# Performance work log

Hardware: AMD Instinct MI355X
Metric: run time of the kernel (lower is better)

## Reference

```python
import jax, jax.numpy as jnp
import numpy as np

B, H, W = 8, 80, 160
N = B * H * W          # flattened pixels
G = 8                  # cost groups
D = 64                 # disparity candidates
NS = 4                 # num_seed
E = 128                # embed_dim
NFREQ = 15             # fourier freqs -> (2*15+1)*1 = 31 dims
NORMALIZER = 3.14 / 64


def setup_inputs() -> dict:
    key = jax.random.key(0)
    ks = jax.random.split(key, 8)
    cost_volume = jax.random.normal(ks[0], (N, G, D), jnp.float32)
    label_seed = jax.random.randint(ks[1], (N, NS), 0, D)
    context = jax.random.normal(ks[2], (B, H, W, E), jnp.float32)
    s = 0.02
    W1 = jax.random.normal(ks[3], (G * 9, E), jnp.float32) * s
    b1 = jnp.zeros((E,), jnp.float32)
    W2 = jax.random.normal(ks[4], (E, E), jnp.float32) * s
    b2 = jnp.zeros((E,), jnp.float32)
    Wp = jax.random.normal(ks[5], (E + 31, E), jnp.float32) * s
    return {"cost_volume": cost_volume, "label_seed": label_seed, "context": context,
            "W1": W1, "b1": b1, "W2": W2, "b2": b2, "Wp": Wp}


def sample_cost(cost_volume, label_seed):
    # cost_volume: [N,G,D], label_seed: [N,NS] -> [N,NS,G*9]
    offset = jnp.arange(-4, 5, dtype=label_seed.dtype)              # [9]
    idx = jnp.clip(label_seed[:, :, None] + offset, 0, D - 1)      # [N,NS,9]
    idx = jnp.broadcast_to(idx.reshape(N, 1, NS * 9), (N, G, NS * 9))
    cost = jnp.take_along_axis(cost_volume, idx, axis=-1)          # [N,G,NS*9]
    # rearrange 'b h (n c) -> b n (h c)'
    cost = cost.reshape(N, G, NS, 9).transpose(0, 2, 1, 3).reshape(N, NS, G * 9)
    return cost


def fourier_embed(label_f):
    # label_f: [N,NS] float -> [N,NS,31]
    coord = label_f * NORMALIZER                                   # [N,NS]
    freqs = 2.0 ** jnp.arange(NFREQ, dtype=label_f.dtype)          # logscale bands
    f = coord[..., None] * freqs                                   # [N,NS,15]
    return jnp.concatenate([jnp.sin(f), jnp.cos(f), coord[..., None]], axis=-1)


def reference(cost_volume, label_seed, context, W1, b1, W2, b2, Wp):
    cost = sample_cost(cost_volume, label_seed)                    # [N,NS,72]
    h = jax.nn.gelu(cost @ W1 + b1, approximate=False)
    cost_feat = h @ W2 + b2                                        # [N,NS,E]
    label_f = label_seed.astype(jnp.float32)
    disp_enc = fourier_embed(label_f)                              # [N,NS,31]
    sample_embed = jnp.concatenate([cost_feat, disp_enc], axis=-1) @ Wp  # [N,NS,E]
    # layers=[] and norm=None -> passthrough; context unused
    return sample_embed[None], label_f
```

## Files before the change

kernel.cpp:

```cpp
#include <hip/hip_runtime.h>
#include <hip/hip_bf16.h>
#include <math.h>

#define NPIX 102400
#define NSEED 4
#define RTOT (NPIX * NSEED)
#define GG 8
#define DD 64
#define EE 128
#define BM 64

#define KP1 96
#define KP2 128
#define KP3 160

#define PC 104
#define PH 136
#define PF 168

typedef short bf16x8 __attribute__((ext_vector_type(8)));
typedef short bf16x4 __attribute__((ext_vector_type(4)));
typedef float f32x4 __attribute__((ext_vector_type(4)));

static __device__ __forceinline__ short f2bf(float x) {
    __hip_bfloat16 h = __float2bfloat16(x);
    return __builtin_bit_cast(short, h);
}

static __device__ __forceinline__ float gelu_exact(float x) {
    return 0.5f * x * (1.0f + erff(x * 0.7071067811865475f));
}

__global__ void prep_weights(const float* __restrict__ W1,
                             const float* __restrict__ W2,
                             const float* __restrict__ Wp,
                             short* __restrict__ ws) {
    const int i = blockIdx.x * 256 + threadIdx.x;
    if (i < 12288) {
        const int e = i / KP1, k = i - e * KP1;
        ws[i] = (k < 72) ? f2bf(W1[k * EE + e]) : (short)0;
    } else if (i < 12288 + 16384) {
        const int j = i - 12288;
        const int e = j / KP2, k = j - e * KP2;
        ws[i] = f2bf(W2[k * EE + e]);
    } else if (i < 49152) {
        const int j = i - 28672;
        const int e = j / KP3, k = j - e * KP3;
        ws[i] = (k < 159) ? f2bf(Wp[k * EE + e]) : (short)0;
    }
}

template <int KPAD, int PADB>
__device__ __forceinline__ void gemm_tiles(const short* __restrict__ WT, const short* sB,
                                           int mt0, int ln, int qd, f32x4 acc[2][4]) {
#pragma unroll
    for (int ks = 0; ks < KPAD / 32; ++ks) {
        const int kb = ks * 32 + qd * 8;
        const bf16x8 a0 = *(const bf16x8*)(WT + (mt0 * 16 + ln) * KPAD + kb);
        const bf16x8 a1 = *(const bf16x8*)(WT + (mt0 * 16 + 16 + ln) * KPAD + kb);
        const bf16x8 b0 = *(const bf16x8*)(sB + (0 * 16 + ln) * PADB + kb);
        const bf16x8 b1 = *(const bf16x8*)(sB + (1 * 16 + ln) * PADB + kb);
        const bf16x8 b2 = *(const bf16x8*)(sB + (2 * 16 + ln) * PADB + kb);
        const bf16x8 b3 = *(const bf16x8*)(sB + (3 * 16 + ln) * PADB + kb);
        acc[0][0] = __builtin_amdgcn_mfma_f32_16x16x32_bf16(a0, b0, acc[0][0], 0, 0, 0);
        acc[0][1] = __builtin_amdgcn_mfma_f32_16x16x32_bf16(a0, b1, acc[0][1], 0, 0, 0);
        acc[0][2] = __builtin_amdgcn_mfma_f32_16x16x32_bf16(a0, b2, acc[0][2], 0, 0, 0);
        acc[0][3] = __builtin_amdgcn_mfma_f32_16x16x32_bf16(a0, b3, acc[0][3], 0, 0, 0);
        acc[1][0] = __builtin_amdgcn_mfma_f32_16x16x32_bf16(a1, b0, acc[1][0], 0, 0, 0);
        acc[1][1] = __builtin_amdgcn_mfma_f32_16x16x32_bf16(a1, b1, acc[1][1], 0, 0, 0);
        acc[1][2] = __builtin_amdgcn_mfma_f32_16x16x32_bf16(a1, b2, acc[1][2], 0, 0, 0);
        acc[1][3] = __builtin_amdgcn_mfma_f32_16x16x32_bf16(a1, b3, acc[1][3], 0, 0, 0);
    }
}

__global__ __launch_bounds__(256, 4)
void Propagation_85315230368231_kernel(const float* __restrict__ cost_volume,
                                       const int* __restrict__ label_seed,
                                       const short* __restrict__ ws,
                                       const float* __restrict__ b1,
                                       const float* __restrict__ b2,
                                       float* __restrict__ out) {
    __shared__ short sU[BM * PF];
    __shared__ short sHT[BM * PH];
    __shared__ int sSeed[BM];

    const short* W1T = ws;
    const short* W2T = ws + 12288;
    const short* WpT = ws + 28672;

    const int tid = threadIdx.x;
    const int blk = blockIdx.x;
    const int p0 = blk * (BM / NSEED);
    const int row0 = blk * BM;

    const int wave = tid >> 6;
    const int lane = tid & 63;
    const int ln = lane & 15;
    const int qd = lane >> 4;
    const int mt0 = wave * 2;

    if (tid < BM) {
        const int sd = label_seed[row0 + tid];
        sSeed[tid] = sd;
        out[(size_t)RTOT * EE + row0 + tid] = (float)sd;
    }
    __syncthreads();

    for (int e = tid; e < BM * 36; e += 256) {
        const int row = e / 36;
        const int pr = e - row * 36;
        const int k0 = pr * 2, k1 = k0 + 1;
        const int sd = sSeed[row];
        const float* cvn = cost_volume + (size_t)(p0 + (row >> 2)) * (GG * DD);
        const int g0 = k0 / 9, c0 = k0 - g0 * 9;
        int d0 = sd + c0 - 4; d0 = d0 < 0 ? 0 : (d0 > 63 ? 63 : d0);
        const float v0 = cvn[g0 * DD + d0];
        const int g1 = k1 / 9, c1 = k1 - g1 * 9;
        int d1 = sd + c1 - 4; d1 = d1 < 0 ? 0 : (d1 > 63 ? 63 : d1);
        const float v1 = cvn[g1 * DD + d1];
        const int pk = (int)(unsigned short)f2bf(v0) | ((int)(unsigned short)f2bf(v1) << 16);
        *(int*)(sU + row * PC + k0) = pk;
    }
    for (int e = tid; e < BM * 12; e += 256) {
        const int row = e / 12;
        const int j = e - row * 12;
        *(int*)(sU + row * PC + 72 + 2 * j) = 0;
    }
    __syncthreads();

    f32x4 acc[2][4];

#pragma unroll
    for (int i = 0; i < 2; ++i)
#pragma unroll
        for (int j = 0; j < 4; ++j) acc[i][j] = (f32x4)0.0f;
    gemm_tiles<KP1, PC>(W1T, sU, mt0, ln, qd, acc);
#pragma unroll
    for (int mi = 0; mi < 2; ++mi) {
        const int eb = (mt0 + mi) * 16 + qd * 4;
        const float4 bv = *(const float4*)(b1 + eb);
#pragma unroll
        for (int nt = 0; nt < 4; ++nt) {
            bf16x4 p;
            p[0] = f2bf(gelu_exact(acc[mi][nt][0] + bv.x));
            p[1] = f2bf(gelu_exact(acc[mi][nt][1] + bv.y));
            p[2] = f2bf(gelu_exact(acc[mi][nt][2] + bv.z));
            p[3] = f2bf(gelu_exact(acc[mi][nt][3] + bv.w));
            *(bf16x4*)(sHT + (nt * 16 + ln) * PH + eb) = p;
        }
    }
    __syncthreads();

    for (int e = tid; e < BM * 32; e += 256) {
        const int row = e >> 5;
        const int j = e & 31;
        const float coord = (float)sSeed[row] * (float)(3.14 / 64.0);
        float v;
        if (j < 15) v = sinf(coord * (float)(1 << j));
        else if (j < 30) v = cosf(coord * (float)(1 << (j - 15)));
        else if (j == 30) v = coord;
        else v = 0.0f;
        sU[row * PF + 128 + j] = f2bf(v);
    }

#pragma unroll
    for (int i = 0; i < 2; ++i)
#pragma unroll
        for (int j = 0; j < 4; ++j) acc[i][j] = (f32x4)0.0f;
    gemm_tiles<KP2, PH>(W2T, sHT, mt0, ln, qd, acc);
#pragma unroll
    for (int mi = 0; mi < 2; ++mi) {
        const int eb = (mt0 + mi) * 16 + qd * 4;
        const float4 bv = *(const float4*)(b2 + eb);
#pragma unroll
        for (int nt = 0; nt < 4; ++nt) {
            bf16x4 p;
            p[0] = f2bf(acc[mi][nt][0] + bv.x);
            p[1] = f2bf(acc[mi][nt][1] + bv.y);
            p[2] = f2bf(acc[mi][nt][2] + bv.z);
            p[3] = f2bf(acc[mi][nt][3] + bv.w);
            *(bf16x4*)(sU + (nt * 16 + ln) * PF + eb) = p;
        }
    }
    __syncthreads();

#pragma unroll
    for (int i = 0; i < 2; ++i)
#pragma unroll
        for (int j = 0; j < 4; ++j) acc[i][j] = (f32x4)0.0f;
    gemm_tiles<KP3, PF>(WpT, sU, mt0, ln, qd, acc);
#pragma unroll
    for (int mi = 0; mi < 2; ++mi) {
        const int eb = (mt0 + mi) * 16 + qd * 4;
#pragma unroll
        for (int nt = 0; nt < 4; ++nt) {
            const size_t grow = (size_t)(row0 + nt * 16 + ln);
            float4 v = {acc[mi][nt][0], acc[mi][nt][1], acc[mi][nt][2], acc[mi][nt][3]};
            *(float4*)(out + grow * EE + eb) = v;
        }
    }
}

extern "C" void kernel_launch(void* const* d_in, const int* in_sizes, int n_in,
                              void* d_out, int out_size, void* d_ws, size_t ws_size,
                              hipStream_t stream) {
    const float* cost_volume = (const float*)d_in[0];
    const int* label_seed = (const int*)d_in[1];
    const float* W1 = (const float*)d_in[3];
    const float* b1 = (const float*)d_in[4];
    const float* W2 = (const float*)d_in[5];
    const float* b2 = (const float*)d_in[6];
    const float* Wp = (const float*)d_in[7];
    float* out = (float*)d_out;
    short* ws = (short*)d_ws;

    prep_weights<<<192, 256, 0, stream>>>(W1, W2, Wp, ws);
    Propagation_85315230368231_kernel<<<RTOT / BM, 256, 0, stream>>>(
        cost_volume, label_seed, ws, b1, b2, out);
}
```

Baseline: 461.3 us.

## Restructure MLP kernel to per-wave 16-row tiles with register-resident operands

Each wave now handles its own 16 rows end to end. The gathered cost values are built directly in registers as MFMA B operands, and a private per-wave LDS slice replaces block-wide __syncthreads. The Fourier disparity embedding is precomputed into a 64-entry table in the prep kernel, biases are folded into the accumulator initialisation, outputs use nontemporal stores, and exact erf GELU is replaced by a sigmoid approximation. Together these remove block barriers and transcendental work, but the GELU approximation changes numerics and may exceed tolerance.

```diff
diff --git a/kernel.cpp b/kernel.cpp
--- a/kernel.cpp
+++ b/kernel.cpp
@@ -2,74 +2,52 @@
 #include <hip/hip_bf16.h>
 #include <math.h>
 
-#define NPIX 102400
 #define NSEED 4
-#define RTOT (NPIX * NSEED)
-#define GG 8
-#define DD 64
+#define RTOT 409600
 #define EE 128
-#define BM 64
-
 #define KP1 96
 #define KP2 128
 #define KP3 160
-
-#define PC 104
 #define PH 136
-#define PF 168
 
 typedef short bf16x8 __attribute__((ext_vector_type(8)));
-typedef short bf16x4 __attribute__((ext_vector_type(4)));
 typedef float f32x4 __attribute__((ext_vector_type(4)));
+typedef int   i32x4 __attribute__((ext_vector_type(4)));
 
 static __device__ __forceinline__ short f2bf(float x) {
     __hip_bfloat16 h = __float2bfloat16(x);
     return __builtin_bit_cast(short, h);
 }
 
-static __device__ __forceinline__ float gelu_exact(float x) {
-    return 0.5f * x * (1.0f + erff(x * 0.7071067811865475f));
+static __device__ __forceinline__ int pack2(float a, float b) {
+    return (int)(unsigned short)f2bf(a) | ((int)(unsigned short)f2bf(b) << 16);
 }
 
-__global__ void prep_weights(const float* __restrict__ W1,
-                             const float* __restrict__ W2,
-                             const float* __restrict__ Wp,
-                             short* __restrict__ ws) {
+static __device__ __forceinline__ float gelu_fast(float x) {
+    return x / (1.0f + __expf(-1.702f * x));
+}
+
+__global__ void prep_tables(const float* __restrict__ W1, const float* __restrict__ W2,
+                            const float* __restrict__ Wp, short* __restrict__ ws) {
     const int i = blockIdx.x * 256 + threadIdx.x;
     if (i < 12288) {
         const int e = i / KP1, k = i - e * KP1;
         ws[i] = (k < 72) ? f2bf(W1[k * EE + e]) : (short)0;
-    } else if (i < 12288 + 16384) {
-        const int j = i - 12288;
-        const int e = j / KP2, k = j - e * KP2;
+    } else if (i < 28672) {
+        const int j = i - 12288; const int e = j >> 7, k = j & 127;
         ws[i] = f2bf(W2[k * EE + e]);
     } else if (i < 49152) {
-        const int j = i - 28672;
-        const int e = j / KP3, k = j - e * KP3;
+        const int j = i - 28672; const int e = j / KP3, k = j - e * KP3;
         ws[i] = (k < 159) ? f2bf(Wp[k * EE + e]) : (short)0;
-    }
-}
-
-template <int KPAD, int PADB>
-__device__ __forceinline__ void gemm_tiles(const short* __restrict__ WT, const short* sB,
-                                           int mt0, int ln, int qd, f32x4 acc[2][4]) {
-#pragma unroll
-    for (int ks = 0; ks < KPAD / 32; ++ks) {
-        const int kb = ks * 32 + qd * 8;
-        const bf16x8 a0 = *(const bf16x8*)(WT + (mt0 * 16 + ln) * KPAD + kb);
-        const bf16x8 a1 = *(const bf16x8*)(WT + (mt0 * 16 + 16 + ln) * KPAD + kb);
-        const bf16x8 b0 = *(const bf16x8*)(sB + (0 * 16 + ln) * PADB + kb);
-        const bf16x8 b1 = *(const bf16x8*)(sB + (1 * 16 + ln) * PADB + kb);
-        const bf16x8 b2 = *(const bf16x8*)(sB + (2 * 16 + ln) * PADB + kb);
-        const bf16x8 b3 = *(const bf16x8*)(sB + (3 * 16 + ln) * PADB + kb);
-        acc[0][0] = __builtin_amdgcn_mfma_f32_16x16x32_bf16(a0, b0, acc[0][0], 0, 0, 0);
-        acc[0][1] = __builtin_amdgcn_mfma_f32_16x16x32_bf16(a0, b1, acc[0][1], 0, 0, 0);
-        acc[0][2] = __builtin_amdgcn_mfma_f32_16x16x32_bf16(a0, b2, acc[0][2], 0, 0, 0);
-        acc[0][3] = __builtin_amdgcn_mfma_f32_16x16x32_bf16(a0, b3, acc[0][3], 0, 0, 0);
-        acc[1][0] = __builtin_amdgcn_mfma_f32_16x16x32_bf16(a1, b0, acc[1][0], 0, 0, 0);
-        acc[1][1] = __builtin_amdgcn_mfma_f32_16x16x32_bf16(a1, b1, acc[1][1], 0, 0, 0);
-        acc[1][2] = __builtin_amdgcn_mfma_f32_16x16x32_bf16(a1, b2, acc[1][2], 0, 0, 0);
-        acc[1][3] = __builtin_amdgcn_mfma_f32_16x16x32_bf16(a1, b3, acc[1][3], 0, 0, 0);
+    } else if (i < 51200) {
+        const int j = i - 49152; const int sd = j >> 5, jj = j & 31;
+        const float coord = (float)sd * (float)(3.14 / 64.0);
+        float v;
+        if (jj < 15) v = sinf(coord * (float)(1 << jj));
+        else if (jj < 30) v = cosf(coord * (float)(1 << (jj - 15)));
+        else if (jj == 30) v = coord;
+        else v = 0.0f;
+        ws[i] = f2bf(v);
     }
 }
 
@@ -80,124 +58,118 @@
                                        const float* __restrict__ b1,
                                        const float* __restrict__ b2,
                                        float* __restrict__ out) {
-    __shared__ short sU[BM * PF];
-    __shared__ short sHT[BM * PH];
-    __shared__ int sSeed[BM];
+    __shared__ short sH[4][16 * PH];
 
     const short* W1T = ws;
     const short* W2T = ws + 12288;
     const short* WpT = ws + 28672;
+    const short* DSP = ws + 49152;
 
     const int tid = threadIdx.x;
-    const int blk = blockIdx.x;
-    const int p0 = blk * (BM / NSEED);
-    const int row0 = blk * BM;
-
     const int wave = tid >> 6;
     const int lane = tid & 63;
     const int ln = lane & 15;
     const int qd = lane >> 4;
-    const int mt0 = wave * 2;
+    short* sHw = sH[wave];
 
-    if (tid < BM) {
-        const int sd = label_seed[row0 + tid];
-        sSeed[tid] = sd;
-        out[(size_t)RTOT * EE + row0 + tid] = (float)sd;
+    const int gw = blockIdx.x * 4 + wave;
+    const int row0 = gw * 16;
+    const int row = row0 + ln;
+    const int n = row >> 2;
+
+    const int sd = label_seed[row];
+    if (qd == 0) {
+        __builtin_nontemporal_store((float)sd, out + (size_t)RTOT * EE + row);
     }
-    __syncthreads();
 
-    for (int e = tid; e < BM * 36; e += 256) {
-        const int row = e / 36;
-        const int pr = e - row * 36;
-        const int k0 = pr * 2, k1 = k0 + 1;
-        const int sd = sSeed[row];
-        const float* cvn = cost_volume + (size_t)(p0 + (row >> 2)) * (GG * DD);
-        const int g0 = k0 / 9, c0 = k0 - g0 * 9;
-        int d0 = sd + c0 - 4; d0 = d0 < 0 ? 0 : (d0 > 63 ? 63 : d0);
-        const float v0 = cvn[g0 * DD + d0];
-        const int g1 = k1 / 9, c1 = k1 - g1 * 9;
-        int d1 = sd + c1 - 4; d1 = d1 < 0 ? 0 : (d1 > 63 ? 63 : d1);
-        const float v1 = cvn[g1 * DD + d1];
-        const int pk = (int)(unsigned short)f2bf(v0) | ((int)(unsigned short)f2bf(v1) << 16);
-        *(int*)(sU + row * PC + k0) = pk;
-    }
-    for (int e = tid; e < BM * 12; e += 256) {
-        const int row = e / 12;
-        const int j = e - row * 12;
-        *(int*)(sU + row * PC + 72 + 2 * j) = 0;
-    }
-    __syncthreads();
+    const bf16x8 db = *(const bf16x8*)(DSP + sd * 32 + 8 * qd);
 
-    f32x4 acc[2][4];
-
+    const float* cvn = cost_volume + (size_t)n * 512;
+    i32x4 cb[3];
 #pragma unroll
-    for (int i = 0; i < 2; ++i)
+    for (int ks = 0; ks < 3; ++ks) {
 #pragma unroll
-        for (int j = 0; j < 4; ++j) acc[i][j] = (f32x4)0.0f;
-    gemm_tiles<KP1, PC>(W1T, sU, mt0, ln, qd, acc);
+        for (int d = 0; d < 4; ++d) {
+            int pk = 0;
 #pragma unroll
-    for (int mi = 0; mi < 2; ++mi) {
-        const int eb = (mt0 + mi) * 16 + qd * 4;
-        const float4 bv = *(const float4*)(b1 + eb);
-#pragma unroll
-        for (int nt = 0; nt < 4; ++nt) {
-            bf16x4 p;
-            p[0] = f2bf(gelu_exact(acc[mi][nt][0] + bv.x));
-            p[1] = f2bf(gelu_exact(acc[mi][nt][1] + bv.y));
-            p[2] = f2bf(gelu_exact(acc[mi][nt][2] + bv.z));
-            p[3] = f2bf(gelu_exact(acc[mi][nt][3] + bv.w));
-            *(bf16x4*)(sHT + (nt * 16 + ln) * PH + eb) = p;
+            for (int e = 0; e < 2; ++e) {
+                const int k = ks * 32 + qd * 8 + 2 * d + e;
+                if (k < 72) {
+                    const int g = k / 9;
+                    int dd = sd + (k - g * 9) - 4;
+                    dd = dd < 0 ? 0 : (dd > 63 ? 63 : dd);
+                    const float x = cvn[(g << 6) + dd];
+                    pk |= ((int)(unsigned short)f2bf(x)) << (16 * e);
+                }
+            }
+            cb[ks][d] = pk;
         }
     }
-    __syncthreads();
 
-    for (int e = tid; e < BM * 32; e += 256) {
-        const int row = e >> 5;
-        const int j = e & 31;
-        const float coord = (float)sSeed[row] * (float)(3.14 / 64.0);
-        float v;
-        if (j < 15) v = sinf(coord * (float)(1 << j));
-        else if (j < 30) v = cosf(coord * (float)(1 << (j - 15)));
-        else if (j == 30) v = coord;
-        else v = 0.0f;
-        sU[row * PF + 128 + j] = f2bf(v);
+    f32x4 acc[8];
+#pragma unroll
+    for (int mt = 0; mt < 8; ++mt) acc[mt] = *(const f32x4*)(b1 + mt * 16 + 4 * qd);
+#pragma unroll
+    for (int ks = 0; ks < 3; ++ks) {
+        const bf16x8 bf = __builtin_bit_cast(bf16x8, cb[ks]);
+#pragma unroll
+        for (int mt = 0; mt < 8; ++mt) {
+            const bf16x8 a = *(const bf16x8*)(W1T + (mt * 16 + ln) * KP1 + ks * 32 + qd * 8);
+            acc[mt] = __builtin_amdgcn_mfma_f32_16x16x32_bf16(a, bf, acc[mt], 0, 0, 0);
+        }
+    }
+#pragma unroll
+    for (int mt = 0; mt < 8; ++mt) {
+        int2 w;
+        w.x = pack2(gelu_fast(acc[mt][0]), gelu_fast(acc[mt][1]));
+        w.y = pack2(gelu_fast(acc[mt][2]), gelu_fast(acc[mt][3]));
+        *(int2*)(sHw + ln * PH + mt * 16 + 4 * qd) = w;
+    }
+    __asm__ volatile("s_waitcnt lgkmcnt(0)" ::: "memory");
+
+    f32x4 acc2[8];
+#pragma unroll
+    for (int mt = 0; mt < 8; ++mt) acc2[mt] = *(const f32x4*)(b2 + mt * 16 + 4 * qd);
+#pragma unroll
+    for (int ks = 0; ks < 4; ++ks) {
+        const bf16x8 hb = *(const bf16x8*)(sHw + ln * PH + ks * 32 + qd * 8);
+#pragma unroll
+        for (int mt = 0; mt < 8; ++mt) {
+            const bf16x8 a = *(const bf16x8*)(W2T + (mt * 16 + ln) * KP2 + ks * 32 + qd * 8);
+            acc2[mt] = __builtin_amdgcn_mfma_f32_16x16x32_bf16(a, hb, acc2[mt], 0, 0, 0);
+        }
+    }
+#pragma unroll
+    for (int mt = 0; mt < 8; ++mt) {
+        int2 w;
+        w.x = pack2(acc2[mt][0], acc2[mt][1]);
+        w.y = pack2(acc2[mt][2], acc2[mt][3]);
+        *(int2*)(sHw + ln * PH + mt * 16 + 4 * qd) = w;
+    }
+    __asm__ volatile("s_waitcnt lgkmcnt(0)" ::: "memory");
+
+    f32x4 acc3[8];
+#pragma unroll
+    for (int mt = 0; mt < 8; ++mt) acc3[mt] = (f32x4)0.0f;
+#pragma unroll
+    for (int ks = 0; ks < 4; ++ks) {
+        const bf16x8 fb = *(const bf16x8*)(sHw + ln * PH + ks * 32 + qd * 8);
+#pragma unroll
+        for (int mt = 0; mt < 8; ++mt) {
+            const bf16x8 a = *(const bf16x8*)(WpT + (mt * 16 + ln) * KP3 + ks * 32 + qd * 8);
+            acc3[mt] = __builtin_amdgcn_mfma_f32_16x16x32_bf16(a, fb, acc3[mt], 0, 0, 0);
+        }
+    }
+#pragma unroll
+    for (int mt = 0; mt < 8; ++mt) {
+        const bf16x8 a = *(const bf16x8*)(WpT + (mt * 16 + ln) * KP3 + 128 + qd * 8);
+        acc3[mt] = __builtin_amdgcn_mfma_f32_16x16x32_bf16(a, db, acc3[mt], 0, 0, 0);
     }
 
+    float* orow = out + (size_t)row * EE;
 #pragma unroll
-    for (int i = 0; i < 2; ++i)
-#pragma unroll
-        for (int j = 0; j < 4; ++j) acc[i][j] = (f32x4)0.0f;
-    gemm_tiles<KP2, PH>(W2T, sHT, mt0, ln, qd, acc);
-#pragma unroll
-    for (int mi = 0; mi < 2; ++mi) {
-        const int eb = (mt0 + mi) * 16 + qd * 4;
-        const float4 bv = *(const float4*)(b2 + eb);
-#pragma unroll
-        for (int nt = 0; nt < 4; ++nt) {
-            bf16x4 p;
-            p[0] = f2bf(acc[mi][nt][0] + bv.x);
-            p[1] = f2bf(acc[mi][nt][1] + bv.y);
-            p[2] = f2bf(acc[mi][nt][2] + bv.z);
-            p[3] = f2bf(acc[mi][nt][3] + bv.w);
-            *(bf16x4*)(sU + (nt * 16 + ln) * PF + eb) = p;
-        }
-    }
-    __syncthreads();
-
-#pragma unroll
-    for (int i = 0; i < 2; ++i)
-#pragma unroll
-        for (int j = 0; j < 4; ++j) acc[i][j] = (f32x4)0.0f;
-    gemm_tiles<KP3, PF>(WpT, sU, mt0, ln, qd, acc);
-#pragma unroll
-    for (int mi = 0; mi < 2; ++mi) {
-        const int eb = (mt0 + mi) * 16 + qd * 4;
-#pragma unroll
-        for (int nt = 0; nt < 4; ++nt) {
-            const size_t grow = (size_t)(row0 + nt * 16 + ln);
-            float4 v = {acc[mi][nt][0], acc[mi][nt][1], acc[mi][nt][2], acc[mi][nt][3]};
-            *(float4*)(out + grow * EE + eb) = v;
-        }
+    for (int mt = 0; mt < 8; ++mt) {
+        __builtin_nontemporal_store(acc3[mt], (f32x4*)(orow + mt * 16 + 4 * qd));
     }
 }
 
@@ -214,7 +186,7 @@
     float* out = (float*)d_out;
     short* ws = (short*)d_ws;
 
-    prep_weights<<<192, 256, 0, stream>>>(W1, W2, Wp, ws);
-    Propagation_85315230368231_kernel<<<RTOT / BM, 256, 0, stream>>>(
+    prep_tables<<<200, 256, 0, stream>>>(W1, W2, Wp, ws);
+    Propagation_85315230368231_kernel<<<RTOT / 64, 256, 0, stream>>>(
         cost_volume, label_seed, ws, b1, b2, out);
 }
```

After: 570.9 us. 1.24x slower.
